# Performance work log

Hardware: AMD Instinct MI355X
Metric: run time of the kernel (lower is better)

Reference implementation:

```python
import jax, jax.numpy as jnp
import numpy as np

D_MODEL = 1024
N_EXPERTS = 8
HIDDEN = 2048
TOP_K = 2


def setup_inputs() -> dict:
    key = jax.random.key(0)
    ks = jax.random.split(key, 5)
    scale_in = 1.0 / np.sqrt(D_MODEL)
    scale_h = 1.0 / np.sqrt(HIDDEN)
    return {
        "x": jax.random.normal(ks[0], (2, 2048, D_MODEL), dtype=jnp.float32),
        "w_router": jax.random.normal(ks[1], (D_MODEL, N_EXPERTS), dtype=jnp.float32) * scale_in,
        "w1": jax.random.normal(ks[2], (N_EXPERTS, D_MODEL, HIDDEN), dtype=jnp.float32) * scale_in,
        "w3": jax.random.normal(ks[3], (N_EXPERTS, D_MODEL, HIDDEN), dtype=jnp.float32) * scale_in,
        "w2": jax.random.normal(ks[4], (N_EXPERTS, HIDDEN, D_MODEL), dtype=jnp.float32) * scale_h,
    }


def reference(x, w_router, w1, w3, w2):
    orig_shape = x.shape
    xt = x.reshape(-1, orig_shape[-1])            # [T, D]
    T = xt.shape[0]

    # Router: linear -> softmax -> top-k (weights = top-k softmax scores)
    logits = xt @ w_router                         # [T, E]
    scores = jax.nn.softmax(logits, axis=-1)       # [T, E]
    top_w, top_idx = jax.lax.top_k(scores, TOP_K)  # [T, K]

    # Dense routing-weight matrix (reference form of dispatch/combine)
    dense_w = jnp.zeros((T, N_EXPERTS), dtype=scores.dtype)
    dense_w = dense_w.at[jnp.arange(T)[:, None], top_idx].set(top_w)  # [T, E]

    # Per-expert SwiGLU MLP over all tokens (dense reference of grouped GEMM)
    h1 = jnp.einsum('td,edh->teh', xt, w1)         # [T, E, H]
    h3 = jnp.einsum('td,edh->teh', xt, w3)
    h = jax.nn.silu(h1) * h3                       # [T, E, H]
    y = jnp.einsum('teh,ehd->ted', h, w2)          # [T, E, D]

    # Combine with routing weights
    out = jnp.einsum('te,ted->td', dense_w, y)     # [T, D]
    return out.reshape(orig_shape)
```

## Files before the change

kernel.cpp:

```cpp
#include <hip/hip_runtime.h>
#include <stdint.h>

#define D_MODEL 1024
#define N_EXP   8
#define HIDDEN  2048
#define TOPK    2

#define BK    64
#define PADM  128
#define NT1   (D_MODEL / BK)
#define NT2   (HIDDEN / BK)
#define G1X   1152
#define G2X   288

typedef short bf16x8 __attribute__((ext_vector_type(8)));
typedef float f32x4 __attribute__((ext_vector_type(4)));

__device__ __forceinline__ unsigned short f2bf(float f) {
    union { float f; unsigned u; } v; v.f = f;
    unsigned r = v.u + 0x7fffu + ((v.u >> 16) & 1u);
    return (unsigned short)(r >> 16);
}

__device__ __forceinline__ float bf2f(unsigned short u) {
    union { unsigned u; float f; } v; v.u = (unsigned)u << 16; return v.f;
}

__device__ __forceinline__ void gload_lds16(const void* g, void* l) {
    __builtin_amdgcn_global_load_lds(
        (const __attribute__((address_space(1))) void*)g,
        (__attribute__((address_space(3))) void*)l, 16, 0, 0);
}

__global__ __launch_bounds__(256) void k_prep(
    const float* __restrict__ x, const float* __restrict__ wr,
    const float* __restrict__ w1, const float* __restrict__ w3, const float* __restrict__ w2,
    unsigned short* __restrict__ xb,
    unsigned short* __restrict__ w13t, unsigned short* __restrict__ w2t,
    int* __restrict__ tok_e, float* __restrict__ tok_w,
    int* __restrict__ counts, int T, int nrouter)
{
    __shared__ unsigned tls[128][32];
    const int bx = blockIdx.x;
    const int tid = threadIdx.x;

    if (bx < nrouter) {
        int t = bx * 4 + (tid >> 6);
        int lane = tid & 63;
        if (t >= T) return;
        const float4* xr = (const float4*)(x + (size_t)t * D_MODEL);
        float acc[N_EXP];
#pragma unroll
        for (int e = 0; e < N_EXP; ++e) acc[e] = 0.f;
#pragma unroll
        for (int j = 0; j < 4; ++j) {
            int c = j * 64 + lane;
            float4 v = xr[c];
            ushort4 pk;
            pk.x = f2bf(v.x); pk.y = f2bf(v.y); pk.z = f2bf(v.z); pk.w = f2bf(v.w);
            *(ushort4*)(xb + (size_t)t * D_MODEL + c * 4) = pk;
            const float4* w4 = (const float4*)(wr + (size_t)c * 4 * N_EXP);
#pragma unroll
            for (int k = 0; k < 4; ++k) {
                float xv = (k == 0) ? v.x : (k == 1) ? v.y : (k == 2) ? v.z : v.w;
                float4 wa = w4[k * 2], wb = w4[k * 2 + 1];
                acc[0] += xv * wa.x; acc[1] += xv * wa.y; acc[2] += xv * wa.z; acc[3] += xv * wa.w;
                acc[4] += xv * wb.x; acc[5] += xv * wb.y; acc[6] += xv * wb.z; acc[7] += xv * wb.w;
            }
        }
#pragma unroll
        for (int off = 32; off > 0; off >>= 1) {
#pragma unroll
            for (int e = 0; e < N_EXP; ++e) acc[e] += __shfl_down(acc[e], off, 64);
        }
        if (lane == 0) {
            float mx = acc[0];
#pragma unroll
            for (int e = 1; e < N_EXP; ++e) mx = fmaxf(mx, acc[e]);
            float p[N_EXP], den = 0.f;
#pragma unroll
            for (int e = 0; e < N_EXP; ++e) { p[e] = __expf(acc[e] - mx); den += p[e]; }
            float inv = 1.f / den;
            int e0 = 0; float v0 = acc[0];
#pragma unroll
            for (int e = 1; e < N_EXP; ++e) if (acc[e] > v0) { v0 = acc[e]; e0 = e; }
            int e1 = -1; float v1 = -1e30f;
#pragma unroll
            for (int e = 0; e < N_EXP; ++e) if (e != e0 && acc[e] > v1) { v1 = acc[e]; e1 = e; }
            tok_e[2 * t] = e0;     tok_w[2 * t] = p[e0] * inv;
            tok_e[2 * t + 1] = e1; tok_w[2 * t + 1] = p[e1] * inv;
            atomicAdd(&counts[e0], 1);
            atomicAdd(&counts[e1], 1);
        }
        return;
    }

    const int b2 = bx - nrouter;
    const int z = b2 >> 8;
    const int inner = b2 & 255;
    const int mat = z >> 3, e = z & 7;
    const float* in; int Rr, Cc;
    if (mat == 0)      { in = w1; Rr = D_MODEL; Cc = HIDDEN; }
    else if (mat == 1) { in = w3; Rr = D_MODEL; Cc = HIDDEN; }
    else               { in = w2; Rr = HIDDEN; Cc = D_MODEL; }
    const size_t eb_in = (size_t)e * Rr * Cc;
    const int ntc = Cc >> 7;
    const int c0 = (inner % ntc) * 128;
    const int r0 = (inner / ntc) * 64;

    const int c4 = tid & 31;
    const int rbase = tid >> 5;
    float4 v[8];
#pragma unroll
    for (int p = 0; p < 8; ++p) {
        int row = p * 8 + rbase;
        v[p] = *(const float4*)(in + eb_in + (size_t)(r0 + row) * Cc + c0 + c4 * 4);
    }
    const unsigned swz = (unsigned)((c4 & 7) << 2);
#pragma unroll
    for (int p = 0; p < 8; ++p) {
        int row = p * 8 + rbase;
        unsigned x01 = (unsigned)f2bf(v[p].x) | ((unsigned)f2bf(v[p].y) << 16);
        unsigned x23 = (unsigned)f2bf(v[p].z) | ((unsigned)f2bf(v[p].w) << 16);
        unsigned p01 = __shfl_xor(x01, 32, 64);
        unsigned p23 = __shfl_xor(x23, 32, 64);
        int rr = row >> 1;
        unsigned col = (unsigned)rr ^ swz;
        if ((row & 1) == 0) {
            tls[c4 * 4 + 0][col] = (x01 & 0xffffu) | (p01 << 16);
            tls[c4 * 4 + 1][col] = (x01 >> 16) | (p01 & 0xffff0000u);
        } else {
            tls[c4 * 4 + 2][col] = (p23 & 0xffffu) | (x23 << 16);
            tls[c4 * 4 + 3][col] = (p23 >> 16) | (x23 & 0xffff0000u);
        }
    }
    __syncthreads();

    if (mat < 2) {
        const size_t eb = (size_t)e * (2 * HIDDEN) * D_MODEL;
        const int moff = mat ? 16 : 0;
#pragma unroll
        for (int p = 0; p < 4; ++p) {
            int li = p * 256 + tid;
            int c = li >> 3;
            int j = li & 7;
            unsigned s2 = (unsigned)(((c >> 2) & 7) << 2);
            uint4 d = *(const uint4*)(&tls[c][(unsigned)(j * 4) ^ s2]);
            int C = c0 + c;
            int r13 = ((C >> 4) << 5) + moff + (C & 15);
            *(uint4*)(&w13t[eb + (size_t)r13 * D_MODEL + r0 + j * 8]) = d;
        }
    } else {
        const size_t eb = (size_t)e * D_MODEL * HIDDEN;
#pragma unroll
        for (int p = 0; p < 4; ++p) {
            int li = p * 256 + tid;
            int c = li >> 3;
            int j = li & 7;
            unsigned s2 = (unsigned)(((c >> 2) & 7) << 2);
            uint4 d = *(const uint4*)(&tls[c][(unsigned)(j * 4) ^ s2]);
            *(uint4*)(&w2t[eb + (size_t)(c0 + c) * HIDDEN + r0 + j * 8]) = d;
        }
    }
}

__global__ void k_scan_scatter(const int* __restrict__ counts,
                               const int* __restrict__ tok_e, const float* __restrict__ tok_w,
                               int* __restrict__ offs,
                               int* __restrict__ row_token, float* __restrict__ row_weight,
                               int* __restrict__ tok_pos, int T) {
    __shared__ int scurs[N_EXP];
    if (threadIdx.x == 0) {
        int s = 0;
        for (int e = 0; e < N_EXP; ++e) {
            offs[e] = s; scurs[e] = s;
            s += ((counts[e] + PADM - 1) / PADM) * PADM;
        }
        offs[N_EXP] = s;
    }
    __syncthreads();
    for (int i = threadIdx.x; i < 2 * T; i += blockDim.x) {
        int e = tok_e[i];
        int pos = atomicAdd(&scurs[e], 1);
        row_token[pos] = i >> 1;
        row_weight[pos] = tok_w[i];
        tok_pos[i] = pos;
    }
}

__global__ __launch_bounds__(512, 1) void k_gemm1(
    const unsigned short* __restrict__ xb,
    const unsigned short* __restrict__ w13t,
    const int* __restrict__ row_token,
    const float* __restrict__ row_weight,
    const int* __restrict__ offs,
    unsigned short* __restrict__ h)
{
    __shared__ unsigned short A[3][128 * BK];
    __shared__ unsigned short B[3][256 * BK];

    const int b = blockIdx.x;
    const int bs = (b & 7) * (G1X / 8) + (b >> 3);
    int e = 0, mt = 0, nt = 0, found = 0, at = 0;
#pragma unroll
    for (int ee = 0; ee < N_EXP; ++ee) {
        int me = (offs[ee + 1] - offs[ee]) >> 7;
        int te = me * 16;
        if (!found && bs < at + te) {
            int loc = bs - at;
            nt = loc / me;
            mt = loc - nt * me;
            e = ee; found = 1;
        }
        at += te;
    }
    if (!found) return;
    const int m0 = offs[e] + mt * 128;
    const int n0b = nt * 256;

    const int tid = threadIdx.x;
    const int lane = tid & 63, wid = tid >> 6;
    const int wm = wid >> 2, wn = wid & 3;

    const unsigned short* asrc[2];
    unsigned aoff[2];
#pragma unroll
    for (int q = 0; q < 2; ++q) {
        int c = q * 512 + tid;
        int m = c >> 3, kc = c & 7;
        int kcs = kc ^ (m & 7);
        int tok = row_token[m0 + m];
        asrc[q] = xb + (size_t)tok * D_MODEL + kcs * 8;
        aoff[q] = (unsigned)c * 8u;
    }
    const unsigned short* bsrc[4];
    unsigned boff[4];
#pragma unroll
    for (int q = 0; q < 4; ++q) {
        int c = q * 512 + tid;
        int n = c >> 3, kc = c & 7;
        int kcs = kc ^ (n & 7);
        bsrc[q] = w13t + ((size_t)e * (2 * HIDDEN) + n0b + n) * D_MODEL + kcs * 8;
        boff[q] = (unsigned)c * 8u;
    }

    f32x4 acc[4][4];
    const f32x4 zf = {0.f, 0.f, 0.f, 0.f};
#pragma unroll
    for (int mi = 0; mi < 4; ++mi)
#pragma unroll
        for (int ni = 0; ni < 4; ++ni) acc[mi][ni] = zf;

#pragma unroll
    for (int t = 0; t < 2; ++t) {
        const int ko = t * BK;
        gload_lds16(asrc[0] + ko, &A[t][aoff[0]]);
        gload_lds16(asrc[1] + ko, &A[t][aoff[1]]);
        gload_lds16(bsrc[0] + ko, &B[t][boff[0]]);
        gload_lds16(bsrc[1] + ko, &B[t][boff[1]]);
        gload_lds16(bsrc[2] + ko, &B[t][boff[2]]);
        gload_lds16(bsrc[3] + ko, &B[t][boff[3]]);
    }

    int cur = 0;
#pragma unroll 1
    for (int kt = 0; kt < NT1; ++kt) {
        if (kt == NT1 - 1) asm volatile("s_waitcnt vmcnt(0)" ::: "memory");
        else               asm volatile("s_waitcnt vmcnt(6)" ::: "memory");
        __builtin_amdgcn_s_barrier();

        unsigned short* Ac = &A[cur][0];
        unsigned short* Bc = &B[cur][0];
        const int nb = (cur + 2 >= 3) ? (cur - 1) : (cur + 2);
        const int ko = (kt + 2) * BK;
        const bool pf = (kt + 2 < NT1);

        {
            bf16x8 a0[4], b0[4];
            int ke = (lane >> 4) * 8;
#pragma unroll
            for (int mi = 0; mi < 4; ++mi) {
                int m = wm * 64 + mi * 16 + (lane & 15);
                a0[mi] = *(const bf16x8*)(&Ac[m * BK + (ke ^ ((m & 7) * 8))]);
            }
#pragma unroll
            for (int ni = 0; ni < 4; ++ni) {
                int n = wn * 64 + ni * 16 + (lane & 15);
                b0[ni] = *(const bf16x8*)(&Bc[n * BK + (ke ^ ((n & 7) * 8))]);
            }
            if (pf) {
                gload_lds16(asrc[0] + ko, &A[nb][aoff[0]]);
                gload_lds16(asrc[1] + ko, &A[nb][aoff[1]]);
                gload_lds16(bsrc[0] + ko, &B[nb][boff[0]]);
            }
            __builtin_amdgcn_s_barrier();
            __builtin_amdgcn_s_setprio(1);
#pragma unroll
            for (int mi = 0; mi < 4; ++mi)
#pragma unroll
                for (int ni = 0; ni < 4; ++ni)
                    acc[mi][ni] = __builtin_amdgcn_mfma_f32_16x16x32_bf16(a0[mi], b0[ni], acc[mi][ni], 0, 0, 0);
            __builtin_amdgcn_s_setprio(0);
        }
        {
            bf16x8 a1[4], b1[4];
            int ke = 32 + (lane >> 4) * 8;
#pragma unroll
            for (int mi = 0; mi < 4; ++mi) {
                int m = wm * 64 + mi * 16 + (lane & 15);
                a1[mi] = *(const bf16x8*)(&Ac[m * BK + (ke ^ ((m & 7) * 8))]);
            }
#pragma unroll
            for (int ni = 0; ni < 4; ++ni) {
                int n = wn * 64 + ni * 16 + (lane & 15);
                b1[ni] = *(const bf16x8*)(&Bc[n * BK + (ke ^ ((n & 7) * 8))]);
            }
            if (pf) {
                gload_lds16(bsrc[1] + ko, &B[nb][boff[1]]);
                gload_lds16(bsrc[2] + ko, &B[nb][boff[2]]);
                gload_lds16(bsrc[3] + ko, &B[nb][boff[3]]);
            }
            __builtin_amdgcn_s_barrier();
            __builtin_amdgcn_s_setprio(1);
#pragma unroll
            for (int mi = 0; mi < 4; ++mi)
#pragma unroll
                for (int ni = 0; ni < 4; ++ni)
                    acc[mi][ni] = __builtin_amdgcn_mfma_f32_16x16x32_bf16(a1[mi], b1[ni], acc[mi][ni], 0, 0, 0);
            __builtin_amdgcn_s_setprio(0);
        }
        cur = (cur == 2) ? 0 : (cur + 1);
    }

    const int g0 = (n0b + wn * 64) >> 5;
#pragma unroll
    for (int mi = 0; mi < 4; ++mi) {
#pragma unroll
        for (int r = 0; r < 4; ++r) {
            int m = wm * 64 + mi * 16 + (lane >> 4) * 4 + r;
            float wgt = row_weight[m0 + m];
            size_t rowbase = (size_t)(m0 + m) * HIDDEN;
#pragma unroll
            for (int p = 0; p < 2; ++p) {
                float v1 = acc[mi][2 * p][r], v3 = acc[mi][2 * p + 1][r];
                float sv = v1 / (1.f + __expf(-v1));
                int hc = (g0 + p) * 16 + (lane & 15);
                h[rowbase + hc] = f2bf(sv * v3 * wgt);
            }
        }
    }
}

__global__ __launch_bounds__(512, 1) void k_gemm2(
    const unsigned short* __restrict__ h,
    const unsigned short* __restrict__ w2t,
    const int* __restrict__ offs,
    unsigned short* __restrict__ y)
{
    __shared__ unsigned short A[3][128 * BK];
    __shared__ unsigned short B[3][256 * BK];

    const int b = blockIdx.x;
    const int bs = (b & 7) * (G2X / 8) + (b >> 3);
    int e = 0, mt = 0, nt = 0, found = 0, at = 0;
#pragma unroll
    for (int ee = 0; ee < N_EXP; ++ee) {
        int me = (offs[ee + 1] - offs[ee]) >> 7;
        int te = me * 4;
        if (!found && bs < at + te) {
            int loc = bs - at;
            nt = loc / me;
            mt = loc - nt * me;
            e = ee; found = 1;
        }
        at += te;
    }
    if (!found) return;
    const int m0 = offs[e] + mt * 128;
    const int n0 = nt * 256;

    const int tid = threadIdx.x;
    const int lane = tid & 63, wid = tid >> 6;
    const int wm = wid >> 2, wn = wid & 3;

    const unsigned short* asrc[2];
    unsigned aoff[2];
#pragma unroll
    for (int q = 0; q < 2; ++q) {
        int c = q * 512 + tid;
        int m = c >> 3, kc = c & 7;
        int kcs = kc ^ (m & 7);
        asrc[q] = h + (size_t)(m0 + m) * HIDDEN + kcs * 8;
        aoff[q] = (unsigned)c * 8u;
    }
    const unsigned short* bsrc[4];
    unsigned boff[4];
#pragma unroll
    for (int q = 0; q < 4; ++q) {
        int c = q * 512 + tid;
        int n = c >> 3, kc = c & 7;
        int kcs = kc ^ (n & 7);
        bsrc[q] = w2t + ((size_t)e * D_MODEL + n0 + n) * HIDDEN + kcs * 8;
        boff[q] = (unsigned)c * 8u;
    }

    f32x4 acc[4][4];
    const f32x4 zf = {0.f, 0.f, 0.f, 0.f};
#pragma unroll
    for (int mi = 0; mi < 4; ++mi)
#pragma unroll
        for (int ni = 0; ni < 4; ++ni) acc[mi][ni] = zf;

#pragma unroll
    for (int t = 0; t < 2; ++t) {
        const int ko = t * BK;
        gload_lds16(asrc[0] + ko, &A[t][aoff[0]]);
        gload_lds16(asrc[1] + ko, &A[t][aoff[1]]);
        gload_lds16(bsrc[0] + ko, &B[t][boff[0]]);
        gload_lds16(bsrc[1] + ko, &B[t][boff[1]]);
        gload_lds16(bsrc[2] + ko, &B[t][boff[2]]);
        gload_lds16(bsrc[3] + ko, &B[t][boff[3]]);
    }

    int cur = 0;
#pragma unroll 1
    for (int kt = 0; kt < NT2; ++kt) {
        if (kt == NT2 - 1) asm volatile("s_waitcnt vmcnt(0)" ::: "memory");
        else               asm volatile("s_waitcnt vmcnt(6)" ::: "memory");
        __builtin_amdgcn_s_barrier();

        unsigned short* Ac = &A[cur][0];
        unsigned short* Bc = &B[cur][0];
        const int nb = (cur + 2 >= 3) ? (cur - 1) : (cur + 2);
        const int ko = (kt + 2) * BK;
        const bool pf = (kt + 2 < NT2);

        {
            bf16x8 a0[4], b0[4];
            int ke = (lane >> 4) * 8;
#pragma unroll
            for (int mi = 0; mi < 4; ++mi) {
                int m = wm * 64 + mi * 16 + (lane & 15);
                a0[mi] = *(const bf16x8*)(&Ac[m * BK + (ke ^ ((m & 7) * 8))]);
            }
#pragma unroll
            for (int ni = 0; ni < 4; ++ni) {
                int n = wn * 64 + ni * 16 + (lane & 15);
                b0[ni] = *(const bf16x8*)(&Bc[n * BK + (ke ^ ((n & 7) * 8))]);
            }
            if (pf) {
                gload_lds16(asrc[0] + ko, &A[nb][aoff[0]]);
                gload_lds16(asrc[1] + ko, &A[nb][aoff[1]]);
                gload_lds16(bsrc[0] + ko, &B[nb][boff[0]]);
            }
            __builtin_amdgcn_s_barrier();
            __builtin_amdgcn_s_setprio(1);
#pragma unroll
            for (int mi = 0; mi < 4; ++mi)
#pragma unroll
                for (int ni = 0; ni < 4; ++ni)
                    acc[mi][ni] = __builtin_amdgcn_mfma_f32_16x16x32_bf16(a0[mi], b0[ni], acc[mi][ni], 0, 0, 0);
            __builtin_amdgcn_s_setprio(0);
        }
        {
            bf16x8 a1[4], b1[4];
            int ke = 32 + (lane >> 4) * 8;
#pragma unroll
            for (int mi = 0; mi < 4; ++mi) {
                int m = wm * 64 + mi * 16 + (lane & 15);
                a1[mi] = *(const bf16x8*)(&Ac[m * BK + (ke ^ ((m & 7) * 8))]);
            }
#pragma unroll
            for (int ni = 0; ni < 4; ++ni) {
                int n = wn * 64 + ni * 16 + (lane & 15);
                b1[ni] = *(const bf16x8*)(&Bc[n * BK + (ke ^ ((n & 7) * 8))]);
            }
            if (pf) {
                gload_lds16(bsrc[1] + ko, &B[nb][boff[1]]);
                gload_lds16(bsrc[2] + ko, &B[nb][boff[2]]);
                gload_lds16(bsrc[3] + ko, &B[nb][boff[3]]);
            }
            __builtin_amdgcn_s_barrier();
            __builtin_amdgcn_s_setprio(1);
#pragma unroll
            for (int mi = 0; mi < 4; ++mi)
#pragma unroll
                for (int ni = 0; ni < 4; ++ni)
                    acc[mi][ni] = __builtin_amdgcn_mfma_f32_16x16x32_bf16(a1[mi], b1[ni], acc[mi][ni], 0, 0, 0);
            __builtin_amdgcn_s_setprio(0);
        }
        cur = (cur == 2) ? 0 : (cur + 1);
    }

#pragma unroll
    for (int mi = 0; mi < 4; ++mi) {
#pragma unroll
        for (int r = 0; r < 4; ++r) {
            int m = wm * 64 + mi * 16 + (lane >> 4) * 4 + r;
            size_t rowbase = (size_t)(m0 + m) * D_MODEL + n0;
#pragma unroll
            for (int ni = 0; ni < 4; ++ni) {
                int n = wn * 64 + ni * 16 + (lane & 15);
                y[rowbase + n] = f2bf(acc[mi][ni][r]);
            }
        }
    }
}

__global__ void k_combine(const unsigned short* __restrict__ y,
                          const int* __restrict__ tok_pos,
                          float* __restrict__ out, int n8) {
    int i = blockIdx.x * blockDim.x + threadIdx.x;
    if (i >= n8) return;
    int t = i >> 7;
    int c = (i & 127) * 8;
    int p0 = tok_pos[2 * t];
    int p1 = tok_pos[2 * t + 1];
    bf16x8 v0 = *(const bf16x8*)(y + (size_t)p0 * D_MODEL + c);
    bf16x8 v1 = *(const bf16x8*)(y + (size_t)p1 * D_MODEL + c);
    float* op = out + (size_t)t * D_MODEL + c;
    float4 o0, o1;
    o0.x = bf2f((unsigned short)v0[0]) + bf2f((unsigned short)v1[0]);
    o0.y = bf2f((unsigned short)v0[1]) + bf2f((unsigned short)v1[1]);
    o0.z = bf2f((unsigned short)v0[2]) + bf2f((unsigned short)v1[2]);
    o0.w = bf2f((unsigned short)v0[3]) + bf2f((unsigned short)v1[3]);
    o1.x = bf2f((unsigned short)v0[4]) + bf2f((unsigned short)v1[4]);
    o1.y = bf2f((unsigned short)v0[5]) + bf2f((unsigned short)v1[5]);
    o1.z = bf2f((unsigned short)v0[6]) + bf2f((unsigned short)v1[6]);
    o1.w = bf2f((unsigned short)v0[7]) + bf2f((unsigned short)v1[7]);
    *(float4*)op = o0;
    *(float4*)(op + 4) = o1;
}

extern "C" void kernel_launch(void* const* d_in, const int* in_sizes, int n_in,
                              void* d_out, int out_size, void* d_ws, size_t ws_size,
                              hipStream_t stream) {
    const float* x  = (const float*)d_in[0];
    const float* wr = (const float*)d_in[1];
    const float* w1 = (const float*)d_in[2];
    const float* w3 = (const float*)d_in[3];
    const float* w2 = (const float*)d_in[4];
    float* out = (float*)d_out;

    const int T = in_sizes[0] / D_MODEL;
    const int Rp = T * TOPK + N_EXP * PADM;

    char* ws = (char*)d_ws;
    size_t o = 0;
    unsigned short* xb   = (unsigned short*)(ws + o); o += (size_t)T * D_MODEL * 2;
    unsigned short* h    = (unsigned short*)(ws + o); o += (size_t)Rp * HIDDEN * 2;
    unsigned short* w13t = (unsigned short*)(ws + o); o += (size_t)N_EXP * 2 * HIDDEN * D_MODEL * 2;
    unsigned short* w2t  = (unsigned short*)(ws + o); o += (size_t)N_EXP * D_MODEL * HIDDEN * 2;
    int*   row_token  = (int*)(ws + o);   o += (size_t)Rp * 4;
    float* row_weight = (float*)(ws + o); o += (size_t)Rp * 4;
    int*   tok_e      = (int*)(ws + o);   o += (size_t)2 * T * 4;
    float* tok_w      = (float*)(ws + o); o += (size_t)2 * T * 4;
    int*   tok_pos    = (int*)(ws + o);   o += (size_t)2 * T * 4;
    int*   counts     = (int*)(ws + o);   o += 16 * 4;
    int*   offs       = (int*)(ws + o);   o += 16 * 4;

    unsigned short* y = w13t;

    hipMemsetAsync(counts, 0, 16 * 4, stream);
    hipMemsetAsync(row_token, 0, (size_t)Rp * 4, stream);
    hipMemsetAsync(row_weight, 0, (size_t)Rp * 4, stream);

    const int nrouter = (T + 3) / 4;
    const int nprep = nrouter + 6144;
    k_prep<<<nprep, 256, 0, stream>>>(x, wr, w1, w3, w2, xb, w13t, w2t,
                                      tok_e, tok_w, counts, T, nrouter);

    k_scan_scatter<<<1, 1024, 0, stream>>>(counts, tok_e, tok_w, offs,
                                           row_token, row_weight, tok_pos, T);

    k_gemm1<<<G1X, 512, 0, stream>>>(xb, w13t, row_token, row_weight, offs, h);
    k_gemm2<<<G2X, 512, 0, stream>>>(h, w2t, offs, y);

    int n8 = T * D_MODEL / 8;
    k_combine<<<(n8 + 255) / 256, 256, 0, stream>>>(y, tok_pos, out, n8);
}
```

Before: 330.9 us.

## Move w2 transpose into gemm1 tail blocks and use nontemporal weight loads

Splits the prep kernel into a router kernel and a w1/w3 transpose kernel. The w2 fp32-to-bf16 transpose now runs as 2048 extra blocks appended to the gemm1 grid, reusing gemm1's LDS, so it can overlap with or fill gaps in the grouped GEMM. Weight conversion loads and stores are now nontemporal to limit cache pollution. The cost is an extra kernel launch, and the gemm1 grid now mixes heterogeneous blocks that may contend with the GEMM for bandwidth and occupancy.

```diff
diff --git a/kernel.cpp b/kernel.cpp
--- a/kernel.cpp
+++ b/kernel.cpp
@@ -11,10 +11,13 @@
 #define NT1   (D_MODEL / BK)
 #define NT2   (HIDDEN / BK)
 #define G1X   1152
+#define G1W2  2048
+#define G1TOT (G1X + G1W2)
 #define G2X   288
 
 typedef short bf16x8 __attribute__((ext_vector_type(8)));
 typedef float f32x4 __attribute__((ext_vector_type(4)));
+typedef unsigned u32x4 __attribute__((ext_vector_type(4)));
 
 __device__ __forceinline__ unsigned short f2bf(float f) {
     union { float f; unsigned u; } v; v.f = f;
@@ -32,96 +35,92 @@
         (__attribute__((address_space(3))) void*)l, 16, 0, 0);
 }
 
-__global__ __launch_bounds__(256) void k_prep(
+__global__ __launch_bounds__(256) void k_pre(
     const float* __restrict__ x, const float* __restrict__ wr,
-    const float* __restrict__ w1, const float* __restrict__ w3, const float* __restrict__ w2,
     unsigned short* __restrict__ xb,
-    unsigned short* __restrict__ w13t, unsigned short* __restrict__ w2t,
     int* __restrict__ tok_e, float* __restrict__ tok_w,
-    int* __restrict__ counts, int T, int nrouter)
+    int* __restrict__ counts, int T)
+{
+    int t = blockIdx.x * 4 + (threadIdx.x >> 6);
+    int lane = threadIdx.x & 63;
+    if (t >= T) return;
+    const float4* xr = (const float4*)(x + (size_t)t * D_MODEL);
+    float acc[N_EXP];
+#pragma unroll
+    for (int e = 0; e < N_EXP; ++e) acc[e] = 0.f;
+#pragma unroll
+    for (int j = 0; j < 4; ++j) {
+        int c = j * 64 + lane;
+        float4 v = xr[c];
+        ushort4 pk;
+        pk.x = f2bf(v.x); pk.y = f2bf(v.y); pk.z = f2bf(v.z); pk.w = f2bf(v.w);
+        *(ushort4*)(xb + (size_t)t * D_MODEL + c * 4) = pk;
+        const float4* w4 = (const float4*)(wr + (size_t)c * 4 * N_EXP);
+#pragma unroll
+        for (int k = 0; k < 4; ++k) {
+            float xv = (k == 0) ? v.x : (k == 1) ? v.y : (k == 2) ? v.z : v.w;
+            float4 wa = w4[k * 2], wb = w4[k * 2 + 1];
+            acc[0] += xv * wa.x; acc[1] += xv * wa.y; acc[2] += xv * wa.z; acc[3] += xv * wa.w;
+            acc[4] += xv * wb.x; acc[5] += xv * wb.y; acc[6] += xv * wb.z; acc[7] += xv * wb.w;
+        }
+    }
+#pragma unroll
+    for (int off = 32; off > 0; off >>= 1) {
+#pragma unroll
+        for (int e = 0; e < N_EXP; ++e) acc[e] += __shfl_down(acc[e], off, 64);
+    }
+    if (lane == 0) {
+        float mx = acc[0];
+#pragma unroll
+        for (int e = 1; e < N_EXP; ++e) mx = fmaxf(mx, acc[e]);
+        float p[N_EXP], den = 0.f;
+#pragma unroll
+        for (int e = 0; e < N_EXP; ++e) { p[e] = __expf(acc[e] - mx); den += p[e]; }
+        float inv = 1.f / den;
+        int e0 = 0; float v0 = acc[0];
+#pragma unroll
+        for (int e = 1; e < N_EXP; ++e) if (acc[e] > v0) { v0 = acc[e]; e0 = e; }
+        int e1 = -1; float v1 = -1e30f;
+#pragma unroll
+        for (int e = 0; e < N_EXP; ++e) if (e != e0 && acc[e] > v1) { v1 = acc[e]; e1 = e; }
+        tok_e[2 * t] = e0;     tok_w[2 * t] = p[e0] * inv;
+        tok_e[2 * t + 1] = e1; tok_w[2 * t + 1] = p[e1] * inv;
+        atomicAdd(&counts[e0], 1);
+        atomicAdd(&counts[e1], 1);
+    }
+}
+
+__global__ __launch_bounds__(256) void k_wt13(
+    const float* __restrict__ w1, const float* __restrict__ w3,
+    unsigned short* __restrict__ w13t)
 {
     __shared__ unsigned tls[128][32];
     const int bx = blockIdx.x;
     const int tid = threadIdx.x;
-
-    if (bx < nrouter) {
-        int t = bx * 4 + (tid >> 6);
-        int lane = tid & 63;
-        if (t >= T) return;
-        const float4* xr = (const float4*)(x + (size_t)t * D_MODEL);
-        float acc[N_EXP];
-#pragma unroll
-        for (int e = 0; e < N_EXP; ++e) acc[e] = 0.f;
-#pragma unroll
-        for (int j = 0; j < 4; ++j) {
-            int c = j * 64 + lane;
-            float4 v = xr[c];
-            ushort4 pk;
-            pk.x = f2bf(v.x); pk.y = f2bf(v.y); pk.z = f2bf(v.z); pk.w = f2bf(v.w);
-            *(ushort4*)(xb + (size_t)t * D_MODEL + c * 4) = pk;
-            const float4* w4 = (const float4*)(wr + (size_t)c * 4 * N_EXP);
-#pragma unroll
-            for (int k = 0; k < 4; ++k) {
-                float xv = (k == 0) ? v.x : (k == 1) ? v.y : (k == 2) ? v.z : v.w;
-                float4 wa = w4[k * 2], wb = w4[k * 2 + 1];
-                acc[0] += xv * wa.x; acc[1] += xv * wa.y; acc[2] += xv * wa.z; acc[3] += xv * wa.w;
-                acc[4] += xv * wb.x; acc[5] += xv * wb.y; acc[6] += xv * wb.z; acc[7] += xv * wb.w;
-            }
-        }
-#pragma unroll
-        for (int off = 32; off > 0; off >>= 1) {
-#pragma unroll
-            for (int e = 0; e < N_EXP; ++e) acc[e] += __shfl_down(acc[e], off, 64);
-        }
-        if (lane == 0) {
-            float mx = acc[0];
-#pragma unroll
-            for (int e = 1; e < N_EXP; ++e) mx = fmaxf(mx, acc[e]);
-            float p[N_EXP], den = 0.f;
-#pragma unroll
-            for (int e = 0; e < N_EXP; ++e) { p[e] = __expf(acc[e] - mx); den += p[e]; }
-            float inv = 1.f / den;
-            int e0 = 0; float v0 = acc[0];
-#pragma unroll
-            for (int e = 1; e < N_EXP; ++e) if (acc[e] > v0) { v0 = acc[e]; e0 = e; }
-            int e1 = -1; float v1 = -1e30f;
-#pragma unroll
-            for (int e = 0; e < N_EXP; ++e) if (e != e0 && acc[e] > v1) { v1 = acc[e]; e1 = e; }
-            tok_e[2 * t] = e0;     tok_w[2 * t] = p[e0] * inv;
-            tok_e[2 * t + 1] = e1; tok_w[2 * t + 1] = p[e1] * inv;
-            atomicAdd(&counts[e0], 1);
-            atomicAdd(&counts[e1], 1);
-        }
-        return;
-    }
-
-    const int b2 = bx - nrouter;
-    const int z = b2 >> 8;
-    const int inner = b2 & 255;
+    const int z = bx >> 8;
+    const int inner = bx & 255;
     const int mat = z >> 3, e = z & 7;
-    const float* in; int Rr, Cc;
-    if (mat == 0)      { in = w1; Rr = D_MODEL; Cc = HIDDEN; }
-    else if (mat == 1) { in = w3; Rr = D_MODEL; Cc = HIDDEN; }
-    else               { in = w2; Rr = HIDDEN; Cc = D_MODEL; }
-    const size_t eb_in = (size_t)e * Rr * Cc;
-    const int ntc = Cc >> 7;
-    const int c0 = (inner % ntc) * 128;
-    const int r0 = (inner / ntc) * 64;
+    const float* in = mat ? w3 : w1;
+    const int Cc = HIDDEN;
+    const size_t eb_in = (size_t)e * D_MODEL * HIDDEN;
+    const int c0 = (inner & 15) * 128;
+    const int r0 = (inner >> 4) * 64;
 
     const int c4 = tid & 31;
     const int rbase = tid >> 5;
-    float4 v[8];
+    f32x4 v[8];
 #pragma unroll
     for (int p = 0; p < 8; ++p) {
         int row = p * 8 + rbase;
-        v[p] = *(const float4*)(in + eb_in + (size_t)(r0 + row) * Cc + c0 + c4 * 4);
+        v[p] = __builtin_nontemporal_load(
+            (const f32x4*)(in + eb_in + (size_t)(r0 + row) * Cc + c0 + c4 * 4));
     }
     const unsigned swz = (unsigned)((c4 & 7) << 2);
 #pragma unroll
     for (int p = 0; p < 8; ++p) {
         int row = p * 8 + rbase;
-        unsigned x01 = (unsigned)f2bf(v[p].x) | ((unsigned)f2bf(v[p].y) << 16);
-        unsigned x23 = (unsigned)f2bf(v[p].z) | ((unsigned)f2bf(v[p].w) << 16);
+        unsigned x01 = (unsigned)f2bf(v[p][0]) | ((unsigned)f2bf(v[p][1]) << 16);
+        unsigned x23 = (unsigned)f2bf(v[p][2]) | ((unsigned)f2bf(v[p][3]) << 16);
         unsigned p01 = __shfl_xor(x01, 32, 64);
         unsigned p23 = __shfl_xor(x23, 32, 64);
         int rr = row >> 1;
@@ -136,31 +135,19 @@
     }
     __syncthreads();
 
-    if (mat < 2) {
-        const size_t eb = (size_t)e * (2 * HIDDEN) * D_MODEL;
-        const int moff = mat ? 16 : 0;
-#pragma unroll
-        for (int p = 0; p < 4; ++p) {
-            int li = p * 256 + tid;
-            int c = li >> 3;
-            int j = li & 7;
-            unsigned s2 = (unsigned)(((c >> 2) & 7) << 2);
-            uint4 d = *(const uint4*)(&tls[c][(unsigned)(j * 4) ^ s2]);
-            int C = c0 + c;
-            int r13 = ((C >> 4) << 5) + moff + (C & 15);
-            *(uint4*)(&w13t[eb + (size_t)r13 * D_MODEL + r0 + j * 8]) = d;
-        }
-    } else {
-        const size_t eb = (size_t)e * D_MODEL * HIDDEN;
-#pragma unroll
-        for (int p = 0; p < 4; ++p) {
-            int li = p * 256 + tid;
-            int c = li >> 3;
-            int j = li & 7;
-            unsigned s2 = (unsigned)(((c >> 2) & 7) << 2);
-            uint4 d = *(const uint4*)(&tls[c][(unsigned)(j * 4) ^ s2]);
-            *(uint4*)(&w2t[eb + (size_t)(c0 + c) * HIDDEN + r0 + j * 8]) = d;
-        }
+    const size_t eb = (size_t)e * (2 * HIDDEN) * D_MODEL;
+    const int moff = mat ? 16 : 0;
+#pragma unroll
+    for (int p = 0; p < 4; ++p) {
+        int li = p * 256 + tid;
+        int c = li >> 3;
+        int j = li & 7;
+        unsigned s2 = (unsigned)(((c >> 2) & 7) << 2);
+        u32x4 d = *(const u32x4*)(&tls[c][(unsigned)(j * 4) ^ s2]);
+        int C = c0 + c;
+        int r13 = ((C >> 4) << 5) + moff + (C & 15);
+        __builtin_nontemporal_store(d,
+            (u32x4*)(&w13t[eb + (size_t)r13 * D_MODEL + r0 + j * 8]));
     }
 }
 
@@ -191,6 +178,8 @@
 __global__ __launch_bounds__(512, 1) void k_gemm1(
     const unsigned short* __restrict__ xb,
     const unsigned short* __restrict__ w13t,
+    const float* __restrict__ w2,
+    unsigned short* __restrict__ w2t,
     const int* __restrict__ row_token,
     const float* __restrict__ row_weight,
     const int* __restrict__ offs,
@@ -199,7 +188,61 @@
     __shared__ unsigned short A[3][128 * BK];
     __shared__ unsigned short B[3][256 * BK];
 
-    const int b = blockIdx.x;
+    const int bxx = blockIdx.x;
+    const int tid = threadIdx.x;
+
+    if (bxx >= G1X) {
+        const int b2 = bxx - G1X;
+        const int e2 = b2 >> 8, inner = b2 & 255;
+        const int Cc = D_MODEL;
+        const size_t eb_in = (size_t)e2 * HIDDEN * D_MODEL;
+        const int c0 = (inner & 7) * 128;
+        const int r0 = (inner >> 3) * 64;
+        unsigned (*tls)[32] = (unsigned(*)[32])&A[0][0];
+
+        const int c4 = tid & 31;
+        const int rbase = tid >> 5;
+        f32x4 v[4];
+#pragma unroll
+        for (int p = 0; p < 4; ++p) {
+            int row = p * 16 + rbase;
+            v[p] = __builtin_nontemporal_load(
+                (const f32x4*)(w2 + eb_in + (size_t)(r0 + row) * Cc + c0 + c4 * 4));
+        }
+        const unsigned swz = (unsigned)((c4 & 7) << 2);
+#pragma unroll
+        for (int p = 0; p < 4; ++p) {
+            int row = p * 16 + rbase;
+            unsigned x01 = (unsigned)f2bf(v[p][0]) | ((unsigned)f2bf(v[p][1]) << 16);
+            unsigned x23 = (unsigned)f2bf(v[p][2]) | ((unsigned)f2bf(v[p][3]) << 16);
+            unsigned p01 = __shfl_xor(x01, 32, 64);
+            unsigned p23 = __shfl_xor(x23, 32, 64);
+            int rr = row >> 1;
+            unsigned col = (unsigned)rr ^ swz;
+            if ((row & 1) == 0) {
+                tls[c4 * 4 + 0][col] = (x01 & 0xffffu) | (p01 << 16);
+                tls[c4 * 4 + 1][col] = (x01 >> 16) | (p01 & 0xffff0000u);
+            } else {
+                tls[c4 * 4 + 2][col] = (p23 & 0xffffu) | (x23 << 16);
+                tls[c4 * 4 + 3][col] = (p23 >> 16) | (x23 & 0xffff0000u);
+            }
+        }
+        __syncthreads();
+        const size_t eb = (size_t)e2 * D_MODEL * HIDDEN;
+#pragma unroll
+        for (int p = 0; p < 2; ++p) {
+            int li = p * 512 + tid;
+            int c = li >> 3;
+            int j = li & 7;
+            unsigned s2 = (unsigned)(((c >> 2) & 7) << 2);
+            u32x4 d = *(const u32x4*)(&tls[c][(unsigned)(j * 4) ^ s2]);
+            __builtin_nontemporal_store(d,
+                (u32x4*)(&w2t[eb + (size_t)(c0 + c) * HIDDEN + r0 + j * 8]));
+        }
+        return;
+    }
+
+    const int b = bxx;
     const int bs = (b & 7) * (G1X / 8) + (b >> 3);
     int e = 0, mt = 0, nt = 0, found = 0, at = 0;
 #pragma unroll
@@ -218,7 +261,6 @@
     const int m0 = offs[e] + mt * 128;
     const int n0b = nt * 256;
 
-    const int tid = threadIdx.x;
     const int lane = tid & 63, wid = tid >> 6;
     const int wm = wid >> 2, wn = wid & 3;
 
@@ -565,15 +607,13 @@
     hipMemsetAsync(row_token, 0, (size_t)Rp * 4, stream);
     hipMemsetAsync(row_weight, 0, (size_t)Rp * 4, stream);
 
-    const int nrouter = (T + 3) / 4;
-    const int nprep = nrouter + 6144;
-    k_prep<<<nprep, 256, 0, stream>>>(x, wr, w1, w3, w2, xb, w13t, w2t,
-                                      tok_e, tok_w, counts, T, nrouter);
+    k_pre<<<(T + 3) / 4, 256, 0, stream>>>(x, wr, xb, tok_e, tok_w, counts, T);
+    k_wt13<<<4096, 256, 0, stream>>>(w1, w3, w13t);
 
     k_scan_scatter<<<1, 1024, 0, stream>>>(counts, tok_e, tok_w, offs,
                                            row_token, row_weight, tok_pos, T);
 
-    k_gemm1<<<G1X, 512, 0, stream>>>(xb, w13t, row_token, row_weight, offs, h);
+    k_gemm1<<<G1TOT, 512, 0, stream>>>(xb, w13t, w2, w2t, row_token, row_weight, offs, h);
     k_gemm2<<<G2X, 512, 0, stream>>>(h, w2t, offs, y);
 
     int n8 = T * D_MODEL / 8;
```

Result: slower. 368.9 us (+11.5%).

## Use 4-wave blocks with BK=32 and 8x4 MFMA tiles in both grouped GEMMs

Applied to the files above, without the earlier changes.

Both grouped GEMM kernels now launch 256 threads (4 waves) instead of 512, with each wave covering all 128 rows and a 64-column slice (8x4 accumulator tiles). The K-tile shrinks from 64 to 32, which halves the LDS footprint so two blocks can reside per CU (launch_bounds 256,2). The LDS swizzle and load mapping are adjusted to match. The aim is more blocks in flight to hide latency, at the cost of twice as many K iterations and barriers and a larger per-wave register footprint.

```diff
diff --git a/kernel.cpp b/kernel.cpp
--- a/kernel.cpp
+++ b/kernel.cpp
@@ -6,7 +6,7 @@
 #define HIDDEN  2048
 #define TOPK    2
 
-#define BK    64
+#define BK    32
 #define PADM  128
 #define NT1   (D_MODEL / BK)
 #define NT2   (HIDDEN / BK)
@@ -15,6 +15,7 @@
 
 typedef short bf16x8 __attribute__((ext_vector_type(8)));
 typedef float f32x4 __attribute__((ext_vector_type(4)));
+typedef unsigned u32x4 __attribute__((ext_vector_type(4)));
 
 __device__ __forceinline__ unsigned short f2bf(float f) {
     union { float f; unsigned u; } v; v.f = f;
@@ -145,10 +146,10 @@
             int c = li >> 3;
             int j = li & 7;
             unsigned s2 = (unsigned)(((c >> 2) & 7) << 2);
-            uint4 d = *(const uint4*)(&tls[c][(unsigned)(j * 4) ^ s2]);
+            u32x4 d = *(const u32x4*)(&tls[c][(unsigned)(j * 4) ^ s2]);
             int C = c0 + c;
             int r13 = ((C >> 4) << 5) + moff + (C & 15);
-            *(uint4*)(&w13t[eb + (size_t)r13 * D_MODEL + r0 + j * 8]) = d;
+            *(u32x4*)(&w13t[eb + (size_t)r13 * D_MODEL + r0 + j * 8]) = d;
         }
     } else {
         const size_t eb = (size_t)e * D_MODEL * HIDDEN;
@@ -158,8 +159,8 @@
             int c = li >> 3;
             int j = li & 7;
             unsigned s2 = (unsigned)(((c >> 2) & 7) << 2);
-            uint4 d = *(const uint4*)(&tls[c][(unsigned)(j * 4) ^ s2]);
-            *(uint4*)(&w2t[eb + (size_t)(c0 + c) * HIDDEN + r0 + j * 8]) = d;
+            u32x4 d = *(const u32x4*)(&tls[c][(unsigned)(j * 4) ^ s2]);
+            *(u32x4*)(&w2t[eb + (size_t)(c0 + c) * HIDDEN + r0 + j * 8]) = d;
         }
     }
 }
@@ -188,7 +189,7 @@
     }
 }
 
-__global__ __launch_bounds__(512, 1) void k_gemm1(
+__global__ __launch_bounds__(256, 2) void k_gemm1(
     const unsigned short* __restrict__ xb,
     const unsigned short* __restrict__ w13t,
     const int* __restrict__ row_token,
@@ -219,16 +220,15 @@
     const int n0b = nt * 256;
 
     const int tid = threadIdx.x;
-    const int lane = tid & 63, wid = tid >> 6;
-    const int wm = wid >> 2, wn = wid & 3;
+    const int lane = tid & 63, wn = tid >> 6;
 
     const unsigned short* asrc[2];
     unsigned aoff[2];
 #pragma unroll
     for (int q = 0; q < 2; ++q) {
-        int c = q * 512 + tid;
-        int m = c >> 3, kc = c & 7;
-        int kcs = kc ^ (m & 7);
+        int c = q * 256 + tid;
+        int m = c >> 2, kc = c & 3;
+        int kcs = kc ^ (m & 3);
         int tok = row_token[m0 + m];
         asrc[q] = xb + (size_t)tok * D_MODEL + kcs * 8;
         aoff[q] = (unsigned)c * 8u;
@@ -237,17 +237,17 @@
     unsigned boff[4];
 #pragma unroll
     for (int q = 0; q < 4; ++q) {
-        int c = q * 512 + tid;
-        int n = c >> 3, kc = c & 7;
-        int kcs = kc ^ (n & 7);
+        int c = q * 256 + tid;
+        int n = c >> 2, kc = c & 3;
+        int kcs = kc ^ (n & 3);
         bsrc[q] = w13t + ((size_t)e * (2 * HIDDEN) + n0b + n) * D_MODEL + kcs * 8;
         boff[q] = (unsigned)c * 8u;
     }
 
-    f32x4 acc[4][4];
+    f32x4 acc[8][4];
     const f32x4 zf = {0.f, 0.f, 0.f, 0.f};
 #pragma unroll
-    for (int mi = 0; mi < 4; ++mi)
+    for (int mi = 0; mi < 8; ++mi)
 #pragma unroll
         for (int ni = 0; ni < 4; ++ni) acc[mi][ni] = zf;
 
@@ -269,75 +269,49 @@
         else               asm volatile("s_waitcnt vmcnt(6)" ::: "memory");
         __builtin_amdgcn_s_barrier();
 
-        unsigned short* Ac = &A[cur][0];
-        unsigned short* Bc = &B[cur][0];
+        const unsigned short* Ac = &A[cur][0];
+        const unsigned short* Bc = &B[cur][0];
         const int nb = (cur + 2 >= 3) ? (cur - 1) : (cur + 2);
         const int ko = (kt + 2) * BK;
         const bool pf = (kt + 2 < NT1);
 
-        {
-            bf16x8 a0[4], b0[4];
-            int ke = (lane >> 4) * 8;
-#pragma unroll
-            for (int mi = 0; mi < 4; ++mi) {
-                int m = wm * 64 + mi * 16 + (lane & 15);
-                a0[mi] = *(const bf16x8*)(&Ac[m * BK + (ke ^ ((m & 7) * 8))]);
-            }
-#pragma unroll
-            for (int ni = 0; ni < 4; ++ni) {
-                int n = wn * 64 + ni * 16 + (lane & 15);
-                b0[ni] = *(const bf16x8*)(&Bc[n * BK + (ke ^ ((n & 7) * 8))]);
-            }
-            if (pf) {
-                gload_lds16(asrc[0] + ko, &A[nb][aoff[0]]);
-                gload_lds16(asrc[1] + ko, &A[nb][aoff[1]]);
-                gload_lds16(bsrc[0] + ko, &B[nb][boff[0]]);
-            }
-            __builtin_amdgcn_s_barrier();
-            __builtin_amdgcn_s_setprio(1);
-#pragma unroll
-            for (int mi = 0; mi < 4; ++mi)
-#pragma unroll
-                for (int ni = 0; ni < 4; ++ni)
-                    acc[mi][ni] = __builtin_amdgcn_mfma_f32_16x16x32_bf16(a0[mi], b0[ni], acc[mi][ni], 0, 0, 0);
-            __builtin_amdgcn_s_setprio(0);
-        }
-        {
-            bf16x8 a1[4], b1[4];
-            int ke = 32 + (lane >> 4) * 8;
-#pragma unroll
-            for (int mi = 0; mi < 4; ++mi) {
-                int m = wm * 64 + mi * 16 + (lane & 15);
-                a1[mi] = *(const bf16x8*)(&Ac[m * BK + (ke ^ ((m & 7) * 8))]);
-            }
-#pragma unroll
-            for (int ni = 0; ni < 4; ++ni) {
-                int n = wn * 64 + ni * 16 + (lane & 15);
-                b1[ni] = *(const bf16x8*)(&Bc[n * BK + (ke ^ ((n & 7) * 8))]);
-            }
-            if (pf) {
-                gload_lds16(bsrc[1] + ko, &B[nb][boff[1]]);
-                gload_lds16(bsrc[2] + ko, &B[nb][boff[2]]);
-                gload_lds16(bsrc[3] + ko, &B[nb][boff[3]]);
-            }
-            __builtin_amdgcn_s_barrier();
-            __builtin_amdgcn_s_setprio(1);
-#pragma unroll
-            for (int mi = 0; mi < 4; ++mi)
-#pragma unroll
-                for (int ni = 0; ni < 4; ++ni)
-                    acc[mi][ni] = __builtin_amdgcn_mfma_f32_16x16x32_bf16(a1[mi], b1[ni], acc[mi][ni], 0, 0, 0);
-            __builtin_amdgcn_s_setprio(0);
-        }
+        bf16x8 a[8], bf[4];
+        const int ke = (lane >> 4) * 8;
+#pragma unroll
+        for (int mi = 0; mi < 8; ++mi) {
+            int m = mi * 16 + (lane & 15);
+            a[mi] = *(const bf16x8*)(&Ac[m * BK + (ke ^ ((m & 3) * 8))]);
+        }
+#pragma unroll
+        for (int ni = 0; ni < 4; ++ni) {
+            int n = wn * 64 + ni * 16 + (lane & 15);
+            bf[ni] = *(const bf16x8*)(&Bc[n * BK + (ke ^ ((n & 3) * 8))]);
+        }
+        if (pf) {
+            gload_lds16(asrc[0] + ko, &A[nb][aoff[0]]);
+            gload_lds16(asrc[1] + ko, &A[nb][aoff[1]]);
+            gload_lds16(bsrc[0] + ko, &B[nb][boff[0]]);
+            gload_lds16(bsrc[1] + ko, &B[nb][boff[1]]);
+            gload_lds16(bsrc[2] + ko, &B[nb][boff[2]]);
+            gload_lds16(bsrc[3] + ko, &B[nb][boff[3]]);
+        }
+        __builtin_amdgcn_s_barrier();
+        __builtin_amdgcn_s_setprio(1);
+#pragma unroll
+        for (int mi = 0; mi < 8; ++mi)
+#pragma unroll
+            for (int ni = 0; ni < 4; ++ni)
+                acc[mi][ni] = __builtin_amdgcn_mfma_f32_16x16x32_bf16(a[mi], bf[ni], acc[mi][ni], 0, 0, 0);
+        __builtin_amdgcn_s_setprio(0);
         cur = (cur == 2) ? 0 : (cur + 1);
     }
 
     const int g0 = (n0b + wn * 64) >> 5;
 #pragma unroll
-    for (int mi = 0; mi < 4; ++mi) {
+    for (int mi = 0; mi < 8; ++mi) {
 #pragma unroll
         for (int r = 0; r < 4; ++r) {
-            int m = wm * 64 + mi * 16 + (lane >> 4) * 4 + r;
+            int m = mi * 16 + (lane >> 4) * 4 + r;
             float wgt = row_weight[m0 + m];
             size_t rowbase = (size_t)(m0 + m) * HIDDEN;
 #pragma unroll
@@ -351,8 +325,8 @@
     }
 }
 
-__global__ __launch_bounds__(512, 1) void k_gemm2(
-    const unsigned short* __restrict__ h,
+__global__ __launch_bounds__(256, 2) void k_gemm2(
+    const unsigned short* __restrict__ hh,
     const unsigned short* __restrict__ w2t,
     const int* __restrict__ offs,
     unsigned short* __restrict__ y)
@@ -380,34 +354,33 @@
     const int n0 = nt * 256;
 
     const int tid = threadIdx.x;
-    const int lane = tid & 63, wid = tid >> 6;
-    const int wm = wid >> 2, wn = wid & 3;
+    const int lane = tid & 63, wn = tid >> 6;
 
     const unsigned short* asrc[2];
     unsigned aoff[2];
 #pragma unroll
     for (int q = 0; q < 2; ++q) {
-        int c = q * 512 + tid;
-        int m = c >> 3, kc = c & 7;
-        int kcs = kc ^ (m & 7);
-        asrc[q] = h + (size_t)(m0 + m) * HIDDEN + kcs * 8;
+        int c = q * 256 + tid;
+        int m = c >> 2, kc = c & 3;
+        int kcs = kc ^ (m & 3);
+        asrc[q] = hh + (size_t)(m0 + m) * HIDDEN + kcs * 8;
         aoff[q] = (unsigned)c * 8u;
     }
     const unsigned short* bsrc[4];
     unsigned boff[4];
 #pragma unroll
     for (int q = 0; q < 4; ++q) {
-        int c = q * 512 + tid;
-        int n = c >> 3, kc = c & 7;
-        int kcs = kc ^ (n & 7);
+        int c = q * 256 + tid;
+        int n = c >> 2, kc = c & 3;
+        int kcs = kc ^ (n & 3);
         bsrc[q] = w2t + ((size_t)e * D_MODEL + n0 + n) * HIDDEN + kcs * 8;
         boff[q] = (unsigned)c * 8u;
     }
 
-    f32x4 acc[4][4];
+    f32x4 acc[8][4];
     const f32x4 zf = {0.f, 0.f, 0.f, 0.f};
 #pragma unroll
-    for (int mi = 0; mi < 4; ++mi)
+    for (int mi = 0; mi < 8; ++mi)
 #pragma unroll
         for (int ni = 0; ni < 4; ++ni) acc[mi][ni] = zf;
 
@@ -429,74 +402,48 @@
         else               asm volatile("s_waitcnt vmcnt(6)" ::: "memory");
         __builtin_amdgcn_s_barrier();
 
-        unsigned short* Ac = &A[cur][0];
-        unsigned short* Bc = &B[cur][0];
+        const unsigned short* Ac = &A[cur][0];
+        const unsigned short* Bc = &B[cur][0];
         const int nb = (cur + 2 >= 3) ? (cur - 1) : (cur + 2);
         const int ko = (kt + 2) * BK;
         const bool pf = (kt + 2 < NT2);
 
-        {
-            bf16x8 a0[4], b0[4];
-            int ke = (lane >> 4) * 8;
-#pragma unroll
-            for (int mi = 0; mi < 4; ++mi) {
-                int m = wm * 64 + mi * 16 + (lane & 15);
-                a0[mi] = *(const bf16x8*)(&Ac[m * BK + (ke ^ ((m & 7) * 8))]);
-            }
-#pragma unroll
-            for (int ni = 0; ni < 4; ++ni) {
-                int n = wn * 64 + ni * 16 + (lane & 15);
-                b0[ni] = *(const bf16x8*)(&Bc[n * BK + (ke ^ ((n & 7) * 8))]);
-            }
-            if (pf) {
-                gload_lds16(asrc[0] + ko, &A[nb][aoff[0]]);
-                gload_lds16(asrc[1] + ko, &A[nb][aoff[1]]);
-                gload_lds16(bsrc[0] + ko, &B[nb][boff[0]]);
-            }
-            __builtin_amdgcn_s_barrier();
-            __builtin_amdgcn_s_setprio(1);
-#pragma unroll
-            for (int mi = 0; mi < 4; ++mi)
-#pragma unroll
-                for (int ni = 0; ni < 4; ++ni)
-                    acc[mi][ni] = __builtin_amdgcn_mfma_f32_16x16x32_bf16(a0[mi], b0[ni], acc[mi][ni], 0, 0, 0);
-            __builtin_amdgcn_s_setprio(0);
-        }
-        {
-            bf16x8 a1[4], b1[4];
-            int ke = 32 + (lane >> 4) * 8;
-#pragma unroll
-            for (int mi = 0; mi < 4; ++mi) {
-                int m = wm * 64 + mi * 16 + (lane & 15);
-                a1[mi] = *(const bf16x8*)(&Ac[m * BK + (ke ^ ((m & 7) * 8))]);
-            }
-#pragma unroll
-            for (int ni = 0; ni < 4; ++ni) {
-                int n = wn * 64 + ni * 16 + (lane & 15);
-                b1[ni] = *(const bf16x8*)(&Bc[n * BK + (ke ^ ((n & 7) * 8))]);
-            }
-            if (pf) {
-                gload_lds16(bsrc[1] + ko, &B[nb][boff[1]]);
-                gload_lds16(bsrc[2] + ko, &B[nb][boff[2]]);
-                gload_lds16(bsrc[3] + ko, &B[nb][boff[3]]);
-            }
-            __builtin_amdgcn_s_barrier();
-            __builtin_amdgcn_s_setprio(1);
-#pragma unroll
-            for (int mi = 0; mi < 4; ++mi)
-#pragma unroll
-                for (int ni = 0; ni < 4; ++ni)
-                    acc[mi][ni] = __builtin_amdgcn_mfma_f32_16x16x32_bf16(a1[mi], b1[ni], acc[mi][ni], 0, 0, 0);
-            __builtin_amdgcn_s_setprio(0);
-        }
+        bf16x8 a[8], bf[4];
+        const int ke = (lane >> 4) * 8;
+#pragma unroll
+        for (int mi = 0; mi < 8; ++mi) {
+            int m = mi * 16 + (lane & 15);
+            a[mi] = *(const bf16x8*)(&Ac[m * BK + (ke ^ ((m & 3) * 8))]);
+        }
+#pragma unroll
+        for (int ni = 0; ni < 4; ++ni) {
+            int n = wn * 64 + ni * 16 + (lane & 15);
+            bf[ni] = *(const bf16x8*)(&Bc[n * BK + (ke ^ ((n & 3) * 8))]);
+        }
+        if (pf) {
+            gload_lds16(asrc[0] + ko, &A[nb][aoff[0]]);
+            gload_lds16(asrc[1] + ko, &A[nb][aoff[1]]);
+            gload_lds16(bsrc[0] + ko, &B[nb][boff[0]]);
+            gload_lds16(bsrc[1] + ko, &B[nb][boff[1]]);
+            gload_lds16(bsrc[2] + ko, &B[nb][boff[2]]);
+            gload_lds16(bsrc[3] + ko, &B[nb][boff[3]]);
+        }
+        __builtin_amdgcn_s_barrier();
+        __builtin_amdgcn_s_setprio(1);
+#pragma unroll
+        for (int mi = 0; mi < 8; ++mi)
+#pragma unroll
+            for (int ni = 0; ni < 4; ++ni)
+                acc[mi][ni] = __builtin_amdgcn_mfma_f32_16x16x32_bf16(a[mi], bf[ni], acc[mi][ni], 0, 0, 0);
+        __builtin_amdgcn_s_setprio(0);
         cur = (cur == 2) ? 0 : (cur + 1);
     }
 
 #pragma unroll
-    for (int mi = 0; mi < 4; ++mi) {
+    for (int mi = 0; mi < 8; ++mi) {
 #pragma unroll
         for (int r = 0; r < 4; ++r) {
-            int m = wm * 64 + mi * 16 + (lane >> 4) * 4 + r;
+            int m = mi * 16 + (lane >> 4) * 4 + r;
             size_t rowbase = (size_t)(m0 + m) * D_MODEL + n0;
 #pragma unroll
             for (int ni = 0; ni < 4; ++ni) {
@@ -573,8 +520,8 @@
     k_scan_scatter<<<1, 1024, 0, stream>>>(counts, tok_e, tok_w, offs,
                                            row_token, row_weight, tok_pos, T);
 
-    k_gemm1<<<G1X, 512, 0, stream>>>(xb, w13t, row_token, row_weight, offs, h);
-    k_gemm2<<<G2X, 512, 0, stream>>>(h, w2t, offs, y);
+    k_gemm1<<<G1X, 256, 0, stream>>>(xb, w13t, row_token, row_weight, offs, h);
+    k_gemm2<<<G2X, 256, 0, stream>>>(h, w2t, offs, y);
 
     int n8 = T * D_MODEL / 8;
     k_combine<<<(n8 + 255) / 256, 256, 0, stream>>>(y, tok_pos, out, n8);
```

Result: faster. 306.4 us (median of 2 runs) (-7.4%).
